# Performance work log

Hardware: AMD Instinct MI355X
Metric: run time of the kernel (lower is better)

## Reference

```python
import jax, jax.numpy as jnp
import numpy as np

N_NODES = 50000
N_EDGES = 800000
IN_C, HID_C, MID_C = 128, 64, 32


def setup_inputs() -> dict:
    key = jax.random.key(0)
    ks = jax.random.split(key, 9)
    x = jax.random.normal(ks[0], (N_NODES, IN_C), dtype=jnp.float32)
    edge_index = jax.random.randint(ks[1], (2, N_EDGES), 0, N_NODES, dtype=jnp.int32)
    def glorot(k, fan_in, fan_out):
        s = jnp.sqrt(6.0 / (fan_in + fan_out))
        return jax.random.uniform(k, (fan_in, fan_out), jnp.float32, -s, s)
    return {
        "x": x,
        "edge_index": edge_index,
        "W1": glorot(ks[2], IN_C, HID_C), "b1": jnp.zeros((HID_C,), jnp.float32),
        "W2": glorot(ks[3], HID_C, MID_C), "b2": jnp.zeros((MID_C,), jnp.float32),
        "W3": glorot(ks[4], MID_C, 1), "b3": jnp.zeros((1,), jnp.float32),
    }


def _gcn_layer(x, src, dst, edge_norm, W, b):
    # linear transform, then normalized gather-scale-scatter aggregation
    h = x @ W                                   # [N, F_out]
    msg = h[src] * edge_norm[:, None]           # [E+N, F_out]
    out = jax.ops.segment_sum(msg, dst, num_segments=x.shape[0])
    return out + b


def reference(x, edge_index, W1, b1, W2, b2, W3, b3):
    n = x.shape[0]
    loop = jnp.arange(n, dtype=edge_index.dtype)
    src = jnp.concatenate([edge_index[0], loop])   # A + I (self loops)
    dst = jnp.concatenate([edge_index[1], loop])
    # symmetric degree normalization D^{-1/2} (A+I) D^{-1/2}
    deg = jax.ops.segment_sum(jnp.ones_like(dst, dtype=x.dtype), dst, num_segments=n)
    dinv = jnp.where(deg > 0, jax.lax.rsqrt(deg), 0.0)
    edge_norm = dinv[src] * dinv[dst]              # [E+N]

    h = jax.nn.relu(_gcn_layer(x, src, dst, edge_norm, W1, b1))
    h = jax.nn.relu(_gcn_layer(h, src, dst, edge_norm, W2, b2))
    h = _gcn_layer(h, src, dst, edge_norm, W3, b3)
    return jnp.squeeze(h, axis=-1)                 # [N]
```

## Files before the change

### kernel.cpp

```cpp
#include <hip/hip_runtime.h>
#include <hip/hip_fp16.h>


#define IN_C 128
#define NPB_SHIFT 8
#define BCAP 5120

static __device__ __forceinline__ float2 up2(unsigned u) {
    __half2 h = *reinterpret_cast<__half2*>(&u);
    return __half22float2(h);
}
static __device__ __forceinline__ unsigned pk2(float a, float b) {
    __half2 h = __floats2half2_rn(a, b);
    return *reinterpret_cast<unsigned*>(&h);
}


__global__ void zero256_kernel(int* __restrict__ p) { p[threadIdx.x] = 0; }


__global__ __launch_bounds__(256) void partition_kernel(
    const int* __restrict__ src, const int* __restrict__ dst,
    int* __restrict__ bucketcur, unsigned* __restrict__ tmp, int n_edges, int nb) {
    constexpr int EPT = 8;
    __shared__ int hist[256];
    __shared__ int excl[256];
    __shared__ int rankc[256];
    __shared__ int gbase[256];
    __shared__ unsigned sorted[256 * EPT];

    const int t = threadIdx.x;
    const int e0 = blockIdx.x * 256 * EPT;
    hist[t] = 0;
    rankc[t] = 0;
    __syncthreads();

    int d[EPT], s[EPT];
#pragma unroll
    for (int i = 0; i < EPT; ++i) {
        const int e = e0 + t + i * 256;
        if (e < n_edges) {
            d[i] = dst[e];
            s[i] = src[e];
            atomicAdd(&hist[d[i] >> NPB_SHIFT], 1);
        } else {
            d[i] = -1;
        }
    }
    __syncthreads();

    const int hv = hist[t];
    excl[t] = hv;
    __syncthreads();
    for (int off = 1; off < 256; off <<= 1) {
        const int u = (t >= off) ? excl[t - off] : 0;
        __syncthreads();
        excl[t] += u;
        __syncthreads();
    }
    const int ex = excl[t] - hv;
    __syncthreads();
    excl[t] = ex;
    if (t < nb && hv > 0) gbase[t] = t * BCAP + atomicAdd(&bucketcur[t], hv);
    __syncthreads();

#pragma unroll
    for (int i = 0; i < EPT; ++i) {
        if (d[i] >= 0) {
            const int b = d[i] >> NPB_SHIFT;
            const int r = atomicAdd(&rankc[b], 1);
            sorted[excl[b] + r] = ((unsigned)d[i] << 16) | (unsigned)s[i];
        }
    }
    __syncthreads();

    const int m = min(256 * EPT, n_edges - e0);
    for (int i = t; i < m; i += 256) {
        const unsigned pk = sorted[i];
        const int b = (int)(pk >> 24);
        tmp[gbase[b] + (i - excl[b])] = pk;
    }
}


__global__ __launch_bounds__(256) void local_fill_kernel(
    const unsigned* __restrict__ tmp, const int* __restrict__ bucketcur,
    int* __restrict__ row_start, int* __restrict__ deg, float* __restrict__ dinv,
    int* __restrict__ esrc, int n_nodes) {
    __shared__ int histl[256];
    __shared__ int excl[256];
    __shared__ int cur[256];
    const int b = blockIdx.x;
    const int base = b * BCAP;
    const int t = threadIdx.x;
    const int m = bucketcur[b];
    histl[t] = 0;
    __syncthreads();

    for (int i = t; i < m; i += 256)
        atomicAdd(&histl[(tmp[base + i] >> 16) & 255u], 1);
    __syncthreads();

    const int hv = histl[t];
    excl[t] = hv;
    __syncthreads();
    for (int off = 1; off < 256; off <<= 1) {
        const int u = (t >= off) ? excl[t - off] : 0;
        __syncthreads();
        excl[t] += u;
        __syncthreads();
    }
    const int rs = base + excl[t] - hv;
    const int node = (b << NPB_SHIFT) + t;
    if (node < n_nodes) {
        row_start[node] = rs;
        deg[node] = hv;
        dinv[node] = rsqrtf((float)hv + 1.0f);
    }
    cur[t] = rs;
    __syncthreads();

    for (int i = t; i < m; i += 256) {
        const unsigned p = tmp[base + i];
        const int pos = atomicAdd(&cur[(p >> 16) & 255u], 1);
        esrc[pos] = (int)(p & 0xFFFFu);
    }
}


__global__ __launch_bounds__(256) void gemm1_kernel(
    const float* __restrict__ x, const float* __restrict__ W,
    const float* __restrict__ dinv, __half* __restrict__ g1h, int n_nodes) {
    constexpr int KDIM = 128, COUT = 64;
    __shared__ float Wl[KDIM * COUT];
    const int tid = threadIdx.x;
#pragma unroll
    for (int i = 0; i < KDIM * COUT / 1024; ++i) {
        const int idx = (i * 256 + tid) * 4;
        *(float4*)&Wl[idx] = *(const float4*)&W[idx];
    }
    __syncthreads();

    const int tx = tid % 16;
    const int ty = tid / 16;
    const int c0 = tx * 4;
    const int n0 = blockIdx.x * 64 + ty * 4;

    const float4* xr[4];
#pragma unroll
    for (int nn = 0; nn < 4; ++nn) {
        const int node = n0 + nn;
        xr[nn] = (const float4*)(x + (size_t)(node < n_nodes ? node : 0) * KDIM);
    }

    float acc[4][4] = {};
#pragma unroll 4
    for (int k4 = 0; k4 < KDIM / 4; ++k4) {
        float4 xv[4], wv[4];
#pragma unroll
        for (int nn = 0; nn < 4; ++nn) xv[nn] = xr[nn][k4];
#pragma unroll
        for (int kk = 0; kk < 4; ++kk)
            wv[kk] = *(const float4*)&Wl[(k4 * 4 + kk) * COUT + c0];
#pragma unroll
        for (int nn = 0; nn < 4; ++nn) {
            const float xs0 = xv[nn].x, xs1 = xv[nn].y, xs2 = xv[nn].z, xs3 = xv[nn].w;
            acc[nn][0] = fmaf(xs0, wv[0].x, fmaf(xs1, wv[1].x, fmaf(xs2, wv[2].x, fmaf(xs3, wv[3].x, acc[nn][0]))));
            acc[nn][1] = fmaf(xs0, wv[0].y, fmaf(xs1, wv[1].y, fmaf(xs2, wv[2].y, fmaf(xs3, wv[3].y, acc[nn][1]))));
            acc[nn][2] = fmaf(xs0, wv[0].z, fmaf(xs1, wv[1].z, fmaf(xs2, wv[2].z, fmaf(xs3, wv[3].z, acc[nn][2]))));
            acc[nn][3] = fmaf(xs0, wv[0].w, fmaf(xs1, wv[1].w, fmaf(xs2, wv[2].w, fmaf(xs3, wv[3].w, acc[nn][3]))));
        }
    }

#pragma unroll
    for (int nn = 0; nn < 4; ++nn) {
        const int node = n0 + nn;
        if (node < n_nodes) {
            const float dv = dinv[node];
            uint2 pk;
            pk.x = pk2(acc[nn][0] * dv, acc[nn][1] * dv);
            pk.y = pk2(acc[nn][2] * dv, acc[nn][3] * dv);
            *(uint2*)&g1h[(size_t)node * COUT + c0] = pk;
        }
    }
}


#define ACC4(v) { float2 f_ = up2((v).x); a0 += f_.x; a1 += f_.y; \
                  f_ = up2((v).y); a2 += f_.x; a3 += f_.y; }

__global__ __launch_bounds__(256) void agg64_kernel(
    const int* __restrict__ row_start, const int* __restrict__ deg,
    const int* __restrict__ esrc, const __half* __restrict__ g1h,
    const float* __restrict__ dinv, const float* __restrict__ b1,
    __half* __restrict__ z1h, int n) {
    const int t = threadIdx.x;
    const int lane = t & 63;
    const int c16 = lane & 15;
    const int node = blockIdx.x * 16 + (t >> 6) * 4 + (lane >> 4);
    if (node >= n) return;
    const uint2* __restrict__ tab = (const uint2*)g1h;
    const int beg = row_start[node];
    const int dg = deg[node];

    float a0 = 0, a1 = 0, a2 = 0, a3 = 0;
    int i = 0;
    if (dg >= 8) {
        int s0 = esrc[beg], s1 = esrc[beg + 1], s2 = esrc[beg + 2], s3 = esrc[beg + 3];
        for (; i + 8 <= dg; i += 4) {
            const int t0 = esrc[beg + i + 4], t1 = esrc[beg + i + 5],
                      t2 = esrc[beg + i + 6], t3 = esrc[beg + i + 7];
            const uint2 v0 = tab[(size_t)s0 * 16 + c16];
            const uint2 v1 = tab[(size_t)s1 * 16 + c16];
            const uint2 v2 = tab[(size_t)s2 * 16 + c16];
            const uint2 v3 = tab[(size_t)s3 * 16 + c16];
            ACC4(v0); ACC4(v1); ACC4(v2); ACC4(v3);
            s0 = t0; s1 = t1; s2 = t2; s3 = t3;
        }
        const uint2 v0 = tab[(size_t)s0 * 16 + c16];
        const uint2 v1 = tab[(size_t)s1 * 16 + c16];
        const uint2 v2 = tab[(size_t)s2 * 16 + c16];
        const uint2 v3 = tab[(size_t)s3 * 16 + c16];
        ACC4(v0); ACC4(v1); ACC4(v2); ACC4(v3);
        i += 4;
    }
    for (; i + 4 <= dg; i += 4) {
        const int s0 = esrc[beg + i], s1 = esrc[beg + i + 1],
                  s2 = esrc[beg + i + 2], s3 = esrc[beg + i + 3];
        const uint2 v0 = tab[(size_t)s0 * 16 + c16];
        const uint2 v1 = tab[(size_t)s1 * 16 + c16];
        const uint2 v2 = tab[(size_t)s2 * 16 + c16];
        const uint2 v3 = tab[(size_t)s3 * 16 + c16];
        ACC4(v0); ACC4(v1); ACC4(v2); ACC4(v3);
    }
    for (; i < dg; ++i) {
        const uint2 v = tab[(size_t)esrc[beg + i] * 16 + c16];
        ACC4(v);
    }

    const float dv = dinv[node];
    const uint2 sv = tab[(size_t)node * 16 + c16];
    const float2 f0 = up2(sv.x), f1 = up2(sv.y);
    const float4 bb = ((const float4*)b1)[c16];
    const float z0 = fmaxf(dv * (a0 + f0.x) + bb.x, 0.0f);
    const float z1 = fmaxf(dv * (a1 + f0.y) + bb.y, 0.0f);
    const float z2 = fmaxf(dv * (a2 + f1.x) + bb.z, 0.0f);
    const float z3 = fmaxf(dv * (a3 + f1.y) + bb.w, 0.0f);
    uint2 o;
    o.x = pk2(z0, z1);
    o.y = pk2(z2, z3);
    ((uint2*)z1h)[(size_t)node * 16 + c16] = o;
}


__global__ __launch_bounds__(256) void gemm2_kernel(
    const __half* __restrict__ z1h, const float* __restrict__ W2,
    const float* __restrict__ dinv, __half* __restrict__ g2h, int n_nodes) {
    __shared__ float Wl[64 * 32];
    const int tid = threadIdx.x;
    {
        const float4* Ws = (const float4*)W2;
        float4* Wd = (float4*)Wl;
        Wd[tid] = Ws[tid];
        Wd[tid + 256] = Ws[tid + 256];
    }
    __syncthreads();

    const int tx = tid & 7;
    const int ty = tid >> 3;
    const int c0 = tx * 4;
    const int n0 = blockIdx.x * 128 + ty * 4;

    const uint2* xr[4];
#pragma unroll
    for (int nn = 0; nn < 4; ++nn) {
        const int node = n0 + nn;
        xr[nn] = (const uint2*)(z1h + (size_t)(node < n_nodes ? node : 0) * 64);
    }

    float acc[4][4] = {};
#pragma unroll 4
    for (int k4 = 0; k4 < 16; ++k4) {
        float4 wv[4];
#pragma unroll
        for (int kk = 0; kk < 4; ++kk)
            wv[kk] = *(const float4*)&Wl[(k4 * 4 + kk) * 32 + c0];
#pragma unroll
        for (int nn = 0; nn < 4; ++nn) {
            const uint2 xv = xr[nn][k4];
            const float2 xlo = up2(xv.x), xhi = up2(xv.y);
            acc[nn][0] = fmaf(xlo.x, wv[0].x, fmaf(xlo.y, wv[1].x, fmaf(xhi.x, wv[2].x, fmaf(xhi.y, wv[3].x, acc[nn][0]))));
            acc[nn][1] = fmaf(xlo.x, wv[0].y, fmaf(xlo.y, wv[1].y, fmaf(xhi.x, wv[2].y, fmaf(xhi.y, wv[3].y, acc[nn][1]))));
            acc[nn][2] = fmaf(xlo.x, wv[0].z, fmaf(xlo.y, wv[1].z, fmaf(xhi.x, wv[2].z, fmaf(xhi.y, wv[3].z, acc[nn][2]))));
            acc[nn][3] = fmaf(xlo.x, wv[0].w, fmaf(xlo.y, wv[1].w, fmaf(xhi.x, wv[2].w, fmaf(xhi.y, wv[3].w, acc[nn][3]))));
        }
    }

#pragma unroll
    for (int nn = 0; nn < 4; ++nn) {
        const int node = n0 + nn;
        if (node < n_nodes) {
            const float dv = dinv[node];
            uint2 o;
            o.x = pk2(acc[nn][0] * dv, acc[nn][1] * dv);
            o.y = pk2(acc[nn][2] * dv, acc[nn][3] * dv);
            *(uint2*)&g2h[(size_t)node * 32 + c0] = o;
        }
    }
}


__global__ __launch_bounds__(256) void agg32_gemm3_kernel(
    const int* __restrict__ row_start, const int* __restrict__ deg,
    const int* __restrict__ esrc, const __half* __restrict__ g2h,
    const float* __restrict__ dinv, const float* __restrict__ b2,
    const float* __restrict__ W3, float* __restrict__ g3, int n) {
    const int t = threadIdx.x;
    const int lane = t & 63;
    const int c8 = lane & 7;
    const int node = blockIdx.x * 32 + (t >> 6) * 8 + (lane >> 3);
    if (node >= n) return;
    const uint2* __restrict__ tab = (const uint2*)g2h;
    const int beg = row_start[node];
    const int dg = deg[node];

    float a0 = 0, a1 = 0, a2 = 0, a3 = 0;
    int i = 0;
    if (dg >= 8) {
        int s0 = esrc[beg], s1 = esrc[beg + 1], s2 = esrc[beg + 2], s3 = esrc[beg + 3];
        for (; i + 8 <= dg; i += 4) {
            const int t0 = esrc[beg + i + 4], t1 = esrc[beg + i + 5],
                      t2 = esrc[beg + i + 6], t3 = esrc[beg + i + 7];
            const uint2 v0 = tab[(size_t)s0 * 8 + c8];
            const uint2 v1 = tab[(size_t)s1 * 8 + c8];
            const uint2 v2 = tab[(size_t)s2 * 8 + c8];
            const uint2 v3 = tab[(size_t)s3 * 8 + c8];
            ACC4(v0); ACC4(v1); ACC4(v2); ACC4(v3);
            s0 = t0; s1 = t1; s2 = t2; s3 = t3;
        }
        const uint2 v0 = tab[(size_t)s0 * 8 + c8];
        const uint2 v1 = tab[(size_t)s1 * 8 + c8];
        const uint2 v2 = tab[(size_t)s2 * 8 + c8];
        const uint2 v3 = tab[(size_t)s3 * 8 + c8];
        ACC4(v0); ACC4(v1); ACC4(v2); ACC4(v3);
        i += 4;
    }
    for (; i + 4 <= dg; i += 4) {
        const int s0 = esrc[beg + i], s1 = esrc[beg + i + 1],
                  s2 = esrc[beg + i + 2], s3 = esrc[beg + i + 3];
        const uint2 v0 = tab[(size_t)s0 * 8 + c8];
        const uint2 v1 = tab[(size_t)s1 * 8 + c8];
        const uint2 v2 = tab[(size_t)s2 * 8 + c8];
        const uint2 v3 = tab[(size_t)s3 * 8 + c8];
        ACC4(v0); ACC4(v1); ACC4(v2); ACC4(v3);
    }
    for (; i < dg; ++i) {
        const uint2 v = tab[(size_t)esrc[beg + i] * 8 + c8];
        ACC4(v);
    }

    const float dv = dinv[node];
    const uint2 sv = tab[(size_t)node * 8 + c8];
    const float2 f0 = up2(sv.x), f1 = up2(sv.y);
    const float4 bb = ((const float4*)b2)[c8];
    const float4 w = ((const float4*)W3)[c8];
    float p = 0.0f;
    p = fmaf(fmaxf(dv * (a0 + f0.x) + bb.x, 0.0f), w.x, p);
    p = fmaf(fmaxf(dv * (a1 + f0.y) + bb.y, 0.0f), w.y, p);
    p = fmaf(fmaxf(dv * (a2 + f1.x) + bb.z, 0.0f), w.z, p);
    p = fmaf(fmaxf(dv * (a3 + f1.y) + bb.w, 0.0f), w.w, p);
    p += __shfl_xor(p, 1);
    p += __shfl_xor(p, 2);
    p += __shfl_xor(p, 4);
    if (c8 == 0) g3[node] = p * dv;
}


__global__ __launch_bounds__(256) void agg_kernel1(
    const int* __restrict__ row_start, const int* __restrict__ deg,
    const int* __restrict__ esrc, const float* __restrict__ g,
    const float* __restrict__ dinv, const float* __restrict__ b3,
    float* __restrict__ out, int n) {
    const int node = blockIdx.x * 32 + (threadIdx.x >> 3);
    if (node >= n) return;
    const int l = threadIdx.x & 7;
    const int beg = row_start[node], end = beg + deg[node];
    float acc = 0.0f;
    for (int e = beg + l; e < end; e += 8)
        acc += g[esrc[e]];
    acc += __shfl_xor(acc, 1);
    acc += __shfl_xor(acc, 2);
    acc += __shfl_xor(acc, 4);
    if (l == 0) out[node] = dinv[node] * (acc + g[node]) + b3[0];
}


extern "C" void kernel_launch(void* const* d_in, const int* in_sizes, int n_in,
                              void* d_out, int out_size, void* d_ws, size_t ws_size,
                              hipStream_t stream) {
    const float* x  = (const float*)d_in[0];
    const int*   ei = (const int*)d_in[1];
    const float* W1 = (const float*)d_in[2];
    const float* b1 = (const float*)d_in[3];
    const float* W2 = (const float*)d_in[4];
    const float* b2 = (const float*)d_in[5];
    const float* W3 = (const float*)d_in[6];
    const float* b3 = (const float*)d_in[7];
    float* out = (float*)d_out;

    const int n_nodes = in_sizes[0] / IN_C;
    const int n_edges = in_sizes[1] / 2;
    const int* src = ei;
    const int* dst = ei + n_edges;
    const int nbuckets = (n_nodes + (1 << NPB_SHIFT) - 1) >> NPB_SHIFT;

    auto align_up = [](size_t v) { return (v + 255) & ~(size_t)255; };
    char* p = (char*)d_ws;
    int*      bucketcur = (int*)p;     p += align_up(256 * 4);
    int*      row_start = (int*)p;     p += align_up((size_t)n_nodes * 4);
    int*      deg       = (int*)p;     p += align_up((size_t)n_nodes * 4);
    float*    dinv      = (float*)p;   p += align_up((size_t)n_nodes * 4);
    int*      esrc      = (int*)p;     p += align_up((size_t)nbuckets * BCAP * 4);
    __half*   g1h       = (__half*)p;  p += align_up((size_t)n_nodes * 64 * 2);
    __half*   z1h       = (__half*)p;  p += align_up((size_t)n_nodes * 64 * 2);
    char* up = p;
    unsigned* tmp       = (unsigned*)up;
    __half*   g2h       = (__half*)up;
    float*    g3        = (float*)(up + align_up((size_t)n_nodes * 32 * 2));
    (void)ws_size; (void)n_in; (void)out_size;

    zero256_kernel<<<1, 256, 0, stream>>>(bucketcur);
    partition_kernel<<<(n_edges + 2047) / 2048, 256, 0, stream>>>(src, dst, bucketcur, tmp, n_edges, nbuckets);
    local_fill_kernel<<<nbuckets, 256, 0, stream>>>(tmp, bucketcur, row_start, deg, dinv, esrc, n_nodes);

    gemm1_kernel<<<(n_nodes + 63) / 64, 256, 0, stream>>>(x, W1, dinv, g1h, n_nodes);
    agg64_kernel<<<(n_nodes + 15) / 16, 256, 0, stream>>>(row_start, deg, esrc, g1h, dinv, b1, z1h, n_nodes);
    gemm2_kernel<<<(n_nodes + 127) / 128, 256, 0, stream>>>(z1h, W2, dinv, g2h, n_nodes);

    agg32_gemm3_kernel<<<(n_nodes + 31) / 32, 256, 0, stream>>>(row_start, deg, esrc, g2h, dinv, b2, W3, g3, n_nodes);

    agg_kernel1<<<(n_nodes + 31) / 32, 256, 0, stream>>>(row_start, deg, esrc, g3, dinv, b3, out, n_nodes);
}
```

Measured before the change: 98.97 us.

## Widen gather loads to 16 bytes, use wave-shuffle scans, stage bucket in LDS

The aggregation kernels now gather 16-byte (8 half) chunks per lane instead of 8-byte chunks, so fewer lanes serve each node and more nodes are handled per block. This cuts the number of memory instructions per gathered row. The block-wide prefix scans in partition and local_fill are replaced by wave shuffle scans plus a small cross-wave fixup, which removes many barriers. local_fill also caches its bucket in LDS so it reads tmp from global memory only once. The trade-offs are more registers per lane for accumulators, fewer lanes sharing each row's latency, and a large LDS buffer that may lower occupancy.

```diff
diff --git a/kernel.cpp b/kernel.cpp
--- a/kernel.cpp
+++ b/kernel.cpp
@@ -14,6 +14,20 @@
     __half2 h = __floats2half2_rn(a, b);
     return *reinterpret_cast<unsigned*>(&h);
 }
+static __device__ __forceinline__ int wave_incl_scan(int v, int lane) {
+#pragma unroll
+    for (int off = 1; off < 64; off <<= 1) {
+        const int u = __shfl_up(v, off);
+        if (lane >= off) v += u;
+    }
+    return v;
+}
+
+#define ACC8(v) { float2 f_; \
+    f_ = up2((v).x); a[0] += f_.x; a[1] += f_.y; \
+    f_ = up2((v).y); a[2] += f_.x; a[3] += f_.y; \
+    f_ = up2((v).z); a[4] += f_.x; a[5] += f_.y; \
+    f_ = up2((v).w); a[6] += f_.x; a[7] += f_.y; }
 
 
 __global__ void zero256_kernel(int* __restrict__ p) { p[threadIdx.x] = 0; }
@@ -27,9 +41,12 @@
     __shared__ int excl[256];
     __shared__ int rankc[256];
     __shared__ int gbase[256];
+    __shared__ int wsum[4];
     __shared__ unsigned sorted[256 * EPT];
 
     const int t = threadIdx.x;
+    const int lane = t & 63;
+    const int w = t >> 6;
     const int e0 = blockIdx.x * 256 * EPT;
     hist[t] = 0;
     rankc[t] = 0;
@@ -50,17 +67,14 @@
     __syncthreads();
 
     const int hv = hist[t];
-    excl[t] = hv;
-    __syncthreads();
-    for (int off = 1; off < 256; off <<= 1) {
-        const int u = (t >= off) ? excl[t - off] : 0;
-        __syncthreads();
-        excl[t] += u;
-        __syncthreads();
-    }
-    const int ex = excl[t] - hv;
-    __syncthreads();
-    excl[t] = ex;
+    const int inc = wave_incl_scan(hv, lane);
+    if (lane == 63) wsum[w] = inc;
+    __syncthreads();
+    int base = 0;
+#pragma unroll
+    for (int i = 0; i < 4; ++i)
+        if (i < w) base += wsum[i];
+    excl[t] = base + inc - hv;
     if (t < nb && hv > 0) gbase[t] = t * BCAP + atomicAdd(&bucketcur[t], hv);
     __syncthreads();
 
@@ -88,29 +102,34 @@
     int* __restrict__ row_start, int* __restrict__ deg, float* __restrict__ dinv,
     int* __restrict__ esrc, int n_nodes) {
     __shared__ int histl[256];
-    __shared__ int excl[256];
     __shared__ int cur[256];
+    __shared__ int wsum[4];
+    __shared__ unsigned eb[BCAP];
     const int b = blockIdx.x;
     const int base = b * BCAP;
     const int t = threadIdx.x;
-    const int m = bucketcur[b];
+    const int lane = t & 63;
+    const int w = t >> 6;
+    const int m = min(bucketcur[b], BCAP);
     histl[t] = 0;
     __syncthreads();
 
-    for (int i = t; i < m; i += 256)
-        atomicAdd(&histl[(tmp[base + i] >> 16) & 255u], 1);
+    for (int i = t; i < m; i += 256) {
+        const unsigned p = tmp[base + i];
+        eb[i] = p;
+        atomicAdd(&histl[(p >> 16) & 255u], 1);
+    }
     __syncthreads();
 
     const int hv = histl[t];
-    excl[t] = hv;
-    __syncthreads();
-    for (int off = 1; off < 256; off <<= 1) {
-        const int u = (t >= off) ? excl[t - off] : 0;
-        __syncthreads();
-        excl[t] += u;
-        __syncthreads();
-    }
-    const int rs = base + excl[t] - hv;
+    const int inc = wave_incl_scan(hv, lane);
+    if (lane == 63) wsum[w] = inc;
+    __syncthreads();
+    int wb = 0;
+#pragma unroll
+    for (int i = 0; i < 4; ++i)
+        if (i < w) wb += wsum[i];
+    const int rs = base + wb + inc - hv;
     const int node = (b << NPB_SHIFT) + t;
     if (node < n_nodes) {
         row_start[node] = rs;
@@ -121,7 +140,7 @@
     __syncthreads();
 
     for (int i = t; i < m; i += 256) {
-        const unsigned p = tmp[base + i];
+        const unsigned p = eb[i];
         const int pos = atomicAdd(&cur[(p >> 16) & 255u], 1);
         esrc[pos] = (int)(p & 0xFFFFu);
     }
@@ -186,9 +205,6 @@
 }
 
 
-#define ACC4(v) { float2 f_ = up2((v).x); a0 += f_.x; a1 += f_.y; \
-                  f_ = up2((v).y); a2 += f_.x; a3 += f_.y; }
-
 __global__ __launch_bounds__(256) void agg64_kernel(
     const int* __restrict__ row_start, const int* __restrict__ deg,
     const int* __restrict__ esrc, const __half* __restrict__ g1h,
@@ -196,60 +212,63 @@
     __half* __restrict__ z1h, int n) {
     const int t = threadIdx.x;
     const int lane = t & 63;
-    const int c16 = lane & 15;
-    const int node = blockIdx.x * 16 + (t >> 6) * 4 + (lane >> 4);
+    const int c4 = lane & 7;
+    const int node = blockIdx.x * 32 + (t >> 6) * 8 + (lane >> 3);
     if (node >= n) return;
-    const uint2* __restrict__ tab = (const uint2*)g1h;
+    const uint4* __restrict__ tab = (const uint4*)g1h;
     const int beg = row_start[node];
     const int dg = deg[node];
 
-    float a0 = 0, a1 = 0, a2 = 0, a3 = 0;
+    float a[8] = {};
     int i = 0;
     if (dg >= 8) {
         int s0 = esrc[beg], s1 = esrc[beg + 1], s2 = esrc[beg + 2], s3 = esrc[beg + 3];
         for (; i + 8 <= dg; i += 4) {
             const int t0 = esrc[beg + i + 4], t1 = esrc[beg + i + 5],
                       t2 = esrc[beg + i + 6], t3 = esrc[beg + i + 7];
-            const uint2 v0 = tab[(size_t)s0 * 16 + c16];
-            const uint2 v1 = tab[(size_t)s1 * 16 + c16];
-            const uint2 v2 = tab[(size_t)s2 * 16 + c16];
-            const uint2 v3 = tab[(size_t)s3 * 16 + c16];
-            ACC4(v0); ACC4(v1); ACC4(v2); ACC4(v3);
+            const uint4 v0 = tab[(size_t)s0 * 8 + c4];
+            const uint4 v1 = tab[(size_t)s1 * 8 + c4];
+            const uint4 v2 = tab[(size_t)s2 * 8 + c4];
+            const uint4 v3 = tab[(size_t)s3 * 8 + c4];
+            ACC8(v0); ACC8(v1); ACC8(v2); ACC8(v3);
             s0 = t0; s1 = t1; s2 = t2; s3 = t3;
         }
-        const uint2 v0 = tab[(size_t)s0 * 16 + c16];
-        const uint2 v1 = tab[(size_t)s1 * 16 + c16];
-        const uint2 v2 = tab[(size_t)s2 * 16 + c16];
-        const uint2 v3 = tab[(size_t)s3 * 16 + c16];
-        ACC4(v0); ACC4(v1); ACC4(v2); ACC4(v3);
+        const uint4 v0 = tab[(size_t)s0 * 8 + c4];
+        const uint4 v1 = tab[(size_t)s1 * 8 + c4];
+        const uint4 v2 = tab[(size_t)s2 * 8 + c4];
+        const uint4 v3 = tab[(size_t)s3 * 8 + c4];
+        ACC8(v0); ACC8(v1); ACC8(v2); ACC8(v3);
         i += 4;
     }
     for (; i + 4 <= dg; i += 4) {
         const int s0 = esrc[beg + i], s1 = esrc[beg + i + 1],
                   s2 = esrc[beg + i + 2], s3 = esrc[beg + i + 3];
-        const uint2 v0 = tab[(size_t)s0 * 16 + c16];
-        const uint2 v1 = tab[(size_t)s1 * 16 + c16];
-        const uint2 v2 = tab[(size_t)s2 * 16 + c16];
-        const uint2 v3 = tab[(size_t)s3 * 16 + c16];
-        ACC4(v0); ACC4(v1); ACC4(v2); ACC4(v3);
+        const uint4 v0 = tab[(size_t)s0 * 8 + c4];
+        const uint4 v1 = tab[(size_t)s1 * 8 + c4];
+        const uint4 v2 = tab[(size_t)s2 * 8 + c4];
+        const uint4 v3 = tab[(size_t)s3 * 8 + c4];
+        ACC8(v0); ACC8(v1); ACC8(v2); ACC8(v3);
     }
     for (; i < dg; ++i) {
-        const uint2 v = tab[(size_t)esrc[beg + i] * 16 + c16];
-        ACC4(v);
+        const uint4 v = tab[(size_t)esrc[beg + i] * 8 + c4];
+        ACC8(v);
     }
 
     const float dv = dinv[node];
-    const uint2 sv = tab[(size_t)node * 16 + c16];
-    const float2 f0 = up2(sv.x), f1 = up2(sv.y);
-    const float4 bb = ((const float4*)b1)[c16];
-    const float z0 = fmaxf(dv * (a0 + f0.x) + bb.x, 0.0f);
-    const float z1 = fmaxf(dv * (a1 + f0.y) + bb.y, 0.0f);
-    const float z2 = fmaxf(dv * (a2 + f1.x) + bb.z, 0.0f);
-    const float z3 = fmaxf(dv * (a3 + f1.y) + bb.w, 0.0f);
-    uint2 o;
-    o.x = pk2(z0, z1);
-    o.y = pk2(z2, z3);
-    ((uint2*)z1h)[(size_t)node * 16 + c16] = o;
+    const uint4 sv = tab[(size_t)node * 8 + c4];
+    const float2 f0 = up2(sv.x), f1 = up2(sv.y), f2 = up2(sv.z), f3 = up2(sv.w);
+    const float4 bb0 = ((const float4*)b1)[c4 * 2];
+    const float4 bb1 = ((const float4*)b1)[c4 * 2 + 1];
+    uint4 o;
+    o.x = pk2(fmaxf(dv * (a[0] + f0.x) + bb0.x, 0.0f),
+              fmaxf(dv * (a[1] + f0.y) + bb0.y, 0.0f));
+    o.y = pk2(fmaxf(dv * (a[2] + f1.x) + bb0.z, 0.0f),
+              fmaxf(dv * (a[3] + f1.y) + bb0.w, 0.0f));
+    o.z = pk2(fmaxf(dv * (a[4] + f2.x) + bb1.x, 0.0f),
+              fmaxf(dv * (a[5] + f2.y) + bb1.y, 0.0f));
+    o.w = pk2(fmaxf(dv * (a[6] + f3.x) + bb1.z, 0.0f),
+              fmaxf(dv * (a[7] + f3.y) + bb1.w, 0.0f));
+    ((uint4*)z1h)[(size_t)node * 8 + c4] = o;
 }
 
 
@@ -317,62 +336,67 @@
     const float* __restrict__ W3, float* __restrict__ g3, int n) {
     const int t = threadIdx.x;
     const int lane = t & 63;
-    const int c8 = lane & 7;
-    const int node = blockIdx.x * 32 + (t >> 6) * 8 + (lane >> 3);
+    const int c2 = lane & 3;
+    const int node = blockIdx.x * 64 + (t >> 6) * 16 + (lane >> 2);
     if (node >= n) return;
-    const uint2* __restrict__ tab = (const uint2*)g2h;
+    const uint4* __restrict__ tab = (const uint4*)g2h;
     const int beg = row_start[node];
     const int dg = deg[node];
 
-    float a0 = 0, a1 = 0, a2 = 0, a3 = 0;
+    float a[8] = {};
     int i = 0;
     if (dg >= 8) {
         int s0 = esrc[beg], s1 = esrc[beg + 1], s2 = esrc[beg + 2], s3 = esrc[beg + 3];
         for (; i + 8 <= dg; i += 4) {
             const int t0 = esrc[beg + i + 4], t1 = esrc[beg + i + 5],
                       t2 = esrc[beg + i + 6], t3 = esrc[beg + i + 7];
-            const uint2 v0 = tab[(size_t)s0 * 8 + c8];
-            const uint2 v1 = tab[(size_t)s1 * 8 + c8];
-            const uint2 v2 = tab[(size_t)s2 * 8 + c8];
-            const uint2 v3 = tab[(size_t)s3 * 8 + c8];
-            ACC4(v0); ACC4(v1); ACC4(v2); ACC4(v3);
+            const uint4 v0 = tab[(size_t)s0 * 4 + c2];
+            const uint4 v1 = tab[(size_t)s1 * 4 + c2];
+            const uint4 v2 = tab[(size_t)s2 * 4 + c2];
+            const uint4 v3 = tab[(size_t)s3 * 4 + c2];
+            ACC8(v0); ACC8(v1); ACC8(v2); ACC8(v3);
             s0 = t0; s1 = t1; s2 = t2; s3 = t3;
         }
-        const uint2 v0 = tab[(size_t)s0 * 8 + c8];
-        const uint2 v1 = tab[(size_t)s1 * 8 + c8];
-        const uint2 v2 = tab[(size_t)s2 * 8 + c8];
-        const uint2 v3 = tab[(size_t)s3 * 8 + c8];
-        ACC4(v0); ACC4(v1); ACC4(v2); ACC4(v3);
+        const uint4 v0 = tab[(size_t)s0 * 4 + c2];
+        const uint4 v1 = tab[(size_t)s1 * 4 + c2];
+        const uint4 v2 = tab[(size_t)s2 * 4 + c2];
+        const uint4 v3 = tab[(size_t)s3 * 4 + c2];
+        ACC8(v0); ACC8(v1); ACC8(v2); ACC8(v3);
         i += 4;
     }
     for (; i + 4 <= dg; i += 4) {
         const int s0 = esrc[beg + i], s1 = esrc[beg + i + 1],
                   s2 = esrc[beg + i + 2], s3 = esrc[beg + i + 3];
-        const uint2 v0 = tab[(size_t)s0 * 8 + c8];
-        const uint2 v1 = tab[(size_t)s1 * 8 + c8];
-        const uint2 v2 = tab[(size_t)s2 * 8 + c8];
-        const uint2 v3 = tab[(size_t)s3 * 8 + c8];
-        ACC4(v0); ACC4(v1); ACC4(v2); ACC4(v3);
+        const uint4 v0 = tab[(size_t)s0 * 4 + c2];
+        const uint4 v1 = tab[(size_t)s1 * 4 + c2];
+        const uint4 v2 = tab[(size_t)s2 * 4 + c2];
+        const uint4 v3 = tab[(size_t)s3 * 4 + c2];
+        ACC8(v0); ACC8(v1); ACC8(v2); ACC8(v3);
     }
     for (; i < dg; ++i) {
-        const uint2 v = tab[(size_t)esrc[beg + i] * 8 + c8];
-        ACC4(v);
+        const uint4 v = tab[(size_t)esrc[beg + i] * 4 + c2];
+        ACC8(v);
     }
 
     const float dv = dinv[node];
-    const uint2 sv = tab[(size_t)node * 8 + c8];
-    const float2 f0 = up2(sv.x), f1 = up2(sv.y);
-    const float4 bb = ((const float4*)b2)[c8];
-    const float4 w = ((const float4*)W3)[c8];
+    const uint4 sv = tab[(size_t)node * 4 + c2];
+    const float2 f0 = up2(sv.x), f1 = up2(sv.y), f2 = up2(sv.z), f3 = up2(sv.w);
+    const float4 bb0 = ((const float4*)b2)[c2 * 2];
+    const float4 bb1 = ((const float4*)b2)[c2 * 2 + 1];
+    const float4 w0 = ((const float4*)W3)[c2 * 2];
+    const float4 w1 = ((const float4*)W3)[c2 * 2 + 1];
     float p = 0.0f;
-    p = fmaf(fmaxf(dv * (a0 + f0.x) + bb.x, 0.0f), w.x, p);
-    p = fmaf(fmaxf(dv * (a1 + f0.y) + bb.y, 0.0f), w.y, p);
-    p = fmaf(fmaxf(dv * (a2 + f1.x) + bb.z, 0.0f), w.z, p);
-    p = fmaf(fmaxf(dv * (a3 + f1.y) + bb.w, 0.0f), w.w, p);
+    p = fmaf(fmaxf(dv * (a[0] + f0.x) + bb0.x, 0.0f), w0.x, p);
+    p = fmaf(fmaxf(dv * (a[1] + f0.y) + bb0.y, 0.0f), w0.y, p);
+    p = fmaf(fmaxf(dv * (a[2] + f1.x) + bb0.z, 0.0f), w0.z, p);
+    p = fmaf(fmaxf(dv * (a[3] + f1.y) + bb0.w, 0.0f), w0.w, p);
+    p = fmaf(fmaxf(dv * (a[4] + f2.x) + bb1.x, 0.0f), w1.x, p);
+    p = fmaf(fmaxf(dv * (a[5] + f2.y) + bb1.y, 0.0f), w1.y, p);
+    p = fmaf(fmaxf(dv * (a[6] + f3.x) + bb1.z, 0.0f), w1.z, p);
+    p = fmaf(fmaxf(dv * (a[7] + f3.y) + bb1.w, 0.0f), w1.w, p);
     p += __shfl_xor(p, 1);
     p += __shfl_xor(p, 2);
-    p += __shfl_xor(p, 4);
-    if (c8 == 0) g3[node] = p * dv;
+    if (c2 == 0) g3[node] = p * dv;
 }
 
 
@@ -434,10 +458,10 @@
     local_fill_kernel<<<nbuckets, 256, 0, stream>>>(tmp, bucketcur, row_start, deg, dinv, esrc, n_nodes);
 
     gemm1_kernel<<<(n_nodes + 63) / 64, 256, 0, stream>>>(x, W1, dinv, g1h, n_nodes);
-    agg64_kernel<<<(n_nodes + 15) / 16, 256, 0, stream>>>(row_start, deg, esrc, g1h, dinv, b1, z1h, n_nodes);
+    agg64_kernel<<<(n_nodes + 31) / 32, 256, 0, stream>>>(row_start, deg, esrc, g1h, dinv, b1, z1h, n_nodes);
     gemm2_kernel<<<(n_nodes + 127) / 128, 256, 0, stream>>>(z1h, W2, dinv, g2h, n_nodes);
 
-    agg32_gemm3_kernel<<<(n_nodes + 31) / 32, 256, 0, stream>>>(row_start, deg, esrc, g2h, dinv, b2, W3, g3, n_nodes);
+    agg32_gemm3_kernel<<<(n_nodes + 63) / 64, 256, 0, stream>>>(row_start, deg, esrc, g2h, dinv, b2, W3, g3, n_nodes);
 
     agg_kernel1<<<(n_nodes + 31) / 32, 256, 0, stream>>>(row_start, deg, esrc, g3, dinv, b3, out, n_nodes);
 }
```

Result: faster. 95.22 us (-3.8%).
